# Kernel optimization log

Measured on AMD Instinct MI355X. Metric: run time of the kernel, lower is better.

Reference implementation:

```python
import jax, jax.numpy as jnp
import numpy as np

DIM = 4096
N_HEADS = 32
N_KV_HEADS = 8
HEAD_DIM = DIM // N_HEADS  # 128
KV_DIM = N_KV_HEADS * HEAD_DIM  # 1024
B, T = 2, 1024


def setup_inputs() -> dict:
    key = jax.random.key(0)
    ks = jax.random.split(key, 5)
    s1 = 1.0 / np.sqrt(DIM)
    return {
        "x": jax.random.normal(ks[0], (B, T, DIM), dtype=jnp.float32),
        "W1": jax.random.uniform(ks[1], (DIM + 2 * KV_DIM, DIM), dtype=jnp.float32, minval=-s1, maxval=s1),
        "b1": jax.random.uniform(ks[2], (DIM + 2 * KV_DIM,), dtype=jnp.float32, minval=-s1, maxval=s1),
        "W2": jax.random.uniform(ks[3], (DIM, DIM), dtype=jnp.float32, minval=-s1, maxval=s1),
        "b2": jax.random.uniform(ks[4], (DIM,), dtype=jnp.float32, minval=-s1, maxval=s1),
    }


def reference(x, W1, b1, W2, b2):
    Bn, Tn, D = x.shape
    G = N_HEADS // N_KV_HEADS
    qkv = x @ W1.T + b1  # [B,T,D+2*KV_DIM]
    q = qkv[:, :, :DIM]
    k = qkv[:, :, DIM:DIM + KV_DIM]
    v = qkv[:, :, DIM + KV_DIM:]
    # Faithful to torch repeat_interleave(G, dim=-1): scalar-level interleave on flat feature dim
    k = jnp.repeat(k, G, axis=-1)  # [B,T,D]
    v = jnp.repeat(v, G, axis=-1)
    q = q.reshape(Bn, Tn, N_HEADS, HEAD_DIM).transpose(0, 2, 1, 3)  # [B,H,T,hd]
    k = k.reshape(Bn, Tn, N_HEADS, HEAD_DIM).transpose(0, 2, 1, 3)
    v = v.reshape(Bn, Tn, N_HEADS, HEAD_DIM).transpose(0, 2, 1, 3)
    scale = 1.0 / jnp.sqrt(jnp.asarray(HEAD_DIM, dtype=x.dtype))
    qk = jnp.einsum('bhqd,bhkd->bhqk', q, k) * scale  # [B,H,T,T]
    causal = jnp.tril(jnp.ones((Tn, Tn), dtype=bool))
    qk = jnp.where(causal[None, None], qk, jnp.asarray(-jnp.inf, dtype=qk.dtype))
    att = jax.nn.softmax(qk, axis=-1)
    out = jnp.einsum('bhqk,bhkd->bhqd', att, v)  # [B,H,T,hd]
    out = out.transpose(0, 2, 1, 3).reshape(Bn, Tn, D)
    return out @ W2.T + b2
```

## Files before the change

kernel.cpp:

```cpp
#include <hip/hip_runtime.h>

#define DIMX  4096
#define NH    32
#define HD    128
#define BB    2
#define TT    1024
#define MROWS (BB*TT)
#define CQKV  3072
#define SCALE_Q 0.12751743f

typedef _Float16 half_t;
typedef __attribute__((ext_vector_type(4))) _Float16 f16x4;
typedef __attribute__((ext_vector_type(8))) _Float16 f16x8;
typedef __attribute__((ext_vector_type(4))) float    f32x4;

__device__ __forceinline__ void async_copy16(const void* gsrc, void* ldst) {
  __builtin_amdgcn_global_load_lds(
      (const __attribute__((address_space(1))) unsigned int*)gsrc,
      (__attribute__((address_space(3))) unsigned int*)ldst,
      16, 0, 0);
}

__global__ __launch_bounds__(256) void cvt_f32_f16_kernel(
    const float4* __restrict__ src, f16x4* __restrict__ dst, int n4) {
  int stride = gridDim.x * blockDim.x;
  for (int i = blockIdx.x * blockDim.x + threadIdx.x; i < n4; i += stride) {
    float4 f = src[i];
    f16x4 h;
    h.x = (_Float16)f.x; h.y = (_Float16)f.y;
    h.z = (_Float16)f.z; h.w = (_Float16)f.w;
    dst[i] = h;
  }
}

__global__ __launch_bounds__(256) void fold_w1_kernel(
    const float* __restrict__ W1, const float* __restrict__ b1,
    half_t* __restrict__ W1f, float* __restrict__ b1f)
{
  long idx = (long)blockIdx.x * 256 + threadIdx.x;
  int row = (int)(idx >> 10);
  int c4  = ((int)idx & 1023) << 2;
  f16x4 h;
  if (row < 1024) {
    const float* s = W1 + ((long)row << 2) * DIMX + c4;
    float4 a = *(const float4*)s;
    float4 b = *(const float4*)(s + DIMX);
    float4 c = *(const float4*)(s + 2 * DIMX);
    float4 d = *(const float4*)(s + 3 * DIMX);
    h.x = (_Float16)((a.x + b.x + c.x + d.x) * SCALE_Q);
    h.y = (_Float16)((a.y + b.y + c.y + d.y) * SCALE_Q);
    h.z = (_Float16)((a.z + b.z + c.z + d.z) * SCALE_Q);
    h.w = (_Float16)((a.w + b.w + c.w + d.w) * SCALE_Q);
    if (c4 == 0) {
      const float* bb = b1 + ((long)row << 2);
      b1f[row] = (bb[0] + bb[1] + bb[2] + bb[3]) * SCALE_Q;
    }
  } else {
    const float* s = W1 + ((long)(row + 3072)) * DIMX + c4;
    float4 a = *(const float4*)s;
    h.x = (_Float16)a.x; h.y = (_Float16)a.y;
    h.z = (_Float16)a.z; h.w = (_Float16)a.w;
    if (c4 == 0) b1f[row] = b1[row + 3072];
  }
  *(f16x4*)&W1f[(long)row * DIMX + c4] = h;
}

__global__ __launch_bounds__(256) void fold_w2_kernel(
    const float* __restrict__ W2, half_t* __restrict__ W2f)
{
  long idx = (long)blockIdx.x * 256 + threadIdx.x;
  int row = (int)(idx >> 8);
  int j4  = ((int)idx & 255) << 2;
  const float* s = W2 + (long)row * DIMX + ((long)j4 << 2);
  float4 a = *(const float4*)s;
  float4 b = *(const float4*)(s + 4);
  float4 c = *(const float4*)(s + 8);
  float4 d = *(const float4*)(s + 12);
  f16x4 h;
  h.x = (_Float16)(a.x + a.y + a.z + a.w);
  h.y = (_Float16)(b.x + b.y + b.z + b.w);
  h.z = (_Float16)(c.x + c.y + c.z + c.w);
  h.w = (_Float16)(d.x + d.y + d.z + d.w);
  *(f16x4*)&W2f[(long)row * 1024 + j4] = h;
}


__global__ __launch_bounds__(256, 3) void gemm_nt_splitk(
    const half_t* __restrict__ A, const half_t* __restrict__ Bw,
    float* __restrict__ Cp0, float* __restrict__ Cp1,
    int M, int N, int K)
{
  __shared__ alignas(16) half_t As[128 * 64];
  __shared__ alignas(16) half_t Bs[128 * 64];

  const int tid  = threadIdx.x;
  const int lane = tid & 63;
  const int w    = tid >> 6;
  const long row0 = (long)blockIdx.y * 128;
  const long col0 = (long)blockIdx.x * 128;
  const int  KH   = K >> 1;
  const long k0   = (long)blockIdx.z * KH;

  const int rr = tid >> 3;
  const int cs = (((tid & 7) ^ (rr & 7)) << 3);
  const half_t* ga[4]; const half_t* gb[4];
#pragma unroll
  for (int i = 0; i < 4; ++i) {
    ga[i] = A  + (row0 + i * 32 + rr) * K + k0 + cs;
    gb[i] = Bw + (col0 + i * 32 + rr) * K + k0 + cs;
  }
  half_t* lds_a = &As[w * 512];
  half_t* lds_b = &Bs[w * 512];

  const int wm = (w >> 1) * 64;
  const int wn = (w & 1) * 64;
  const int fr   = lane & 15;
  const int quad = lane >> 4;
  const int rsw  = fr & 7;
  const int o0 = ((quad ^ rsw) << 3);
  const int o1 = (((quad | 4) ^ rsw) << 3);
  const half_t* paw = &As[(wm + fr) * 64];
  const half_t* pbw = &Bs[(wn + fr) * 64];

  f32x4 acc[4][4] = {};

  for (int kt = 0; kt < KH; kt += 64) {
    __syncthreads();
#pragma unroll
    for (int i = 0; i < 4; ++i) async_copy16(ga[i] + kt, lds_a + i * 2048);
#pragma unroll
    for (int i = 0; i < 4; ++i) async_copy16(gb[i] + kt, lds_b + i * 2048);
    __syncthreads();

    f16x8 af[4], bf[4];
#pragma unroll
    for (int mi = 0; mi < 4; ++mi) af[mi] = *(const f16x8*)(paw + mi * 1024 + o0);
#pragma unroll
    for (int ni = 0; ni < 4; ++ni) bf[ni] = *(const f16x8*)(pbw + ni * 1024 + o0);
#pragma unroll
    for (int mi = 0; mi < 4; ++mi)
#pragma unroll
      for (int ni = 0; ni < 4; ++ni)
        acc[mi][ni] = __builtin_amdgcn_mfma_f32_16x16x32_f16(
            af[mi], bf[ni], acc[mi][ni], 0, 0, 0);

#pragma unroll
    for (int mi = 0; mi < 4; ++mi) af[mi] = *(const f16x8*)(paw + mi * 1024 + o1);
#pragma unroll
    for (int ni = 0; ni < 4; ++ni) bf[ni] = *(const f16x8*)(pbw + ni * 1024 + o1);
#pragma unroll
    for (int mi = 0; mi < 4; ++mi)
#pragma unroll
      for (int ni = 0; ni < 4; ++ni)
        acc[mi][ni] = __builtin_amdgcn_mfma_f32_16x16x32_f16(
            af[mi], bf[ni], acc[mi][ni], 0, 0, 0);
  }

  float* Cp = blockIdx.z ? Cp1 : Cp0;
  const int er = (lane >> 4) * 4;
  const int ec = lane & 15;
#pragma unroll
  for (int mi = 0; mi < 4; ++mi) {
#pragma unroll
    for (int ni = 0; ni < 4; ++ni) {
      long gn = col0 + wn + ni * 16 + ec;
#pragma unroll
      for (int r = 0; r < 4; ++r) {
        long gm = row0 + wm + mi * 16 + er + r;
        Cp[gm * N + gn] = acc[mi][ni][r];
      }
    }
  }
}

template<int OUT_IS_F16>
__global__ __launch_bounds__(256, 3) void gemm_nt_bias(
    const half_t* __restrict__ A, const half_t* __restrict__ Bw,
    const float* __restrict__ bias, void* __restrict__ Cout,
    int M, int N, int K)
{
  __shared__ alignas(16) half_t As[128 * 64];
  __shared__ alignas(16) half_t Bs[128 * 64];

  const int tid  = threadIdx.x;
  const int lane = tid & 63;
  const int w    = tid >> 6;
  const long row0 = (long)blockIdx.y * 128;
  const long col0 = (long)blockIdx.x * 128;

  const int rr = tid >> 3;
  const int cs = (((tid & 7) ^ (rr & 7)) << 3);
  const half_t* ga[4]; const half_t* gb[4];
#pragma unroll
  for (int i = 0; i < 4; ++i) {
    ga[i] = A  + (row0 + i * 32 + rr) * K + cs;
    gb[i] = Bw + (col0 + i * 32 + rr) * K + cs;
  }
  half_t* lds_a = &As[w * 512];
  half_t* lds_b = &Bs[w * 512];

  const int wm = (w >> 1) * 64;
  const int wn = (w & 1) * 64;
  const int fr   = lane & 15;
  const int quad = lane >> 4;
  const int rsw  = fr & 7;
  const int o0 = ((quad ^ rsw) << 3);
  const int o1 = (((quad | 4) ^ rsw) << 3);
  const half_t* paw = &As[(wm + fr) * 64];
  const half_t* pbw = &Bs[(wn + fr) * 64];

  f32x4 acc[4][4] = {};

  for (int kt = 0; kt < K; kt += 64) {
    __syncthreads();
#pragma unroll
    for (int i = 0; i < 4; ++i) async_copy16(ga[i] + kt, lds_a + i * 2048);
#pragma unroll
    for (int i = 0; i < 4; ++i) async_copy16(gb[i] + kt, lds_b + i * 2048);
    __syncthreads();

    f16x8 af[4], bf[4];
#pragma unroll
    for (int mi = 0; mi < 4; ++mi) af[mi] = *(const f16x8*)(paw + mi * 1024 + o0);
#pragma unroll
    for (int ni = 0; ni < 4; ++ni) bf[ni] = *(const f16x8*)(pbw + ni * 1024 + o0);
#pragma unroll
    for (int mi = 0; mi < 4; ++mi)
#pragma unroll
      for (int ni = 0; ni < 4; ++ni)
        acc[mi][ni] = __builtin_amdgcn_mfma_f32_16x16x32_f16(
            af[mi], bf[ni], acc[mi][ni], 0, 0, 0);

#pragma unroll
    for (int mi = 0; mi < 4; ++mi) af[mi] = *(const f16x8*)(paw + mi * 1024 + o1);
#pragma unroll
    for (int ni = 0; ni < 4; ++ni) bf[ni] = *(const f16x8*)(pbw + ni * 1024 + o1);
#pragma unroll
    for (int mi = 0; mi < 4; ++mi)
#pragma unroll
      for (int ni = 0; ni < 4; ++ni)
        acc[mi][ni] = __builtin_amdgcn_mfma_f32_16x16x32_f16(
            af[mi], bf[ni], acc[mi][ni], 0, 0, 0);
  }

  const int er = (lane >> 4) * 4;
  const int ec = lane & 15;
#pragma unroll
  for (int mi = 0; mi < 4; ++mi) {
#pragma unroll
    for (int ni = 0; ni < 4; ++ni) {
      long gn = col0 + wn + ni * 16 + ec;
      float bv = bias[gn];
#pragma unroll
      for (int r = 0; r < 4; ++r) {
        long gm = row0 + wm + mi * 16 + er + r;
        float v = acc[mi][ni][r] + bv;
        if (OUT_IS_F16) ((half_t*)Cout)[gm * N + gn] = (half_t)v;
        else            ((float*)Cout)[gm * N + gn]  = v;
      }
    }
  }
}

__global__ __launch_bounds__(256) void splitk_reduce_kernel(
    const float4* __restrict__ C0, const float4* __restrict__ C1,
    const float4* __restrict__ bias4, f16x4* __restrict__ dst)
{
  const int col  = blockIdx.x * 256 + threadIdx.x;
  const long row = blockIdx.y;
  const long i   = row * (CQKV / 4) + col;
  float4 a = C0[i];
  float4 b = C1[i];
  float4 bv = bias4[col];
  f16x4 h;
  h.x = (_Float16)(a.x + b.x + bv.x);
  h.y = (_Float16)(a.y + b.y + bv.y);
  h.z = (_Float16)(a.z + b.z + bv.z);
  h.w = (_Float16)(a.w + b.w + bv.w);
  dst[i] = h;
}

#define VTS 72
#define PSS 72
__global__ __launch_bounds__(256, 4) void attn_kernel(
    const half_t* __restrict__ qkv,
    half_t* __restrict__ attc)
{
  __shared__ alignas(16) half_t Ks[64 * 32];
  __shared__ alignas(16) half_t Vt[48 * VTS];
  __shared__ alignas(16) half_t Ps[4][16 * PSS];

  const int tid  = threadIdx.x;
  const int lane = tid & 63;
  const int w    = tid >> 6;
  const int low  = lane & 15;
  const int quad = lane >> 4;
  const int bh   = blockIdx.y;
  const int b    = bh >> 5;
  const int h    = bh & 31;
  const long rb  = (long)b * TT;

  if (tid < 8) {
    f16x8 one;
#pragma unroll
    for (int i = 0; i < 8; ++i) one[i] = (_Float16)1.0f;
    *(f16x8*)&Vt[32 * VTS + tid * 8] = one;
  }

  const int srow = tid >> 2;
  const int sc4  = (tid & 3) << 3;
  half_t* ksdst  = &Ks[w * 512];
  half_t* psw    = &Ps[w][0];
  float*  Ob     = (float*)psw;

  const int tile = blockIdx.x;
  const int t0   = tile * 64;
  const int qg   = t0 + 16 * w;

  f16x8 qf = *(const f16x8*)&qkv[(rb + qg + low) * CQKV + h * 32 + quad * 8];

  f32x4 acc0 = {}, acc1 = {}, acc2 = {};
  const f32x4 zero = {};

  for (int c = 0; c <= t0; c += 64) {
    __syncthreads();
    const half_t* kg = &qkv[(rb + c + srow) * CQKV + 1024 + h * 32 + sc4];
    async_copy16(kg, ksdst);
    f16x8 vv = *(const f16x8*)(kg + 1024);
#pragma unroll
    for (int j = 0; j < 8; ++j)
      Vt[(sc4 + j) * VTS + srow] = vv[j];
    __syncthreads();

    f32x4 s[4];
#pragma unroll
    for (int st = 0; st < 4; ++st) {
      f16x8 kf = *(const f16x8*)&Ks[(st * 16 + low) * 32 + quad * 8];
      s[st] = __builtin_amdgcn_mfma_f32_16x16x32_f16(qf, kf, zero, 0, 0, 0);
    }

    const bool diag = (c == t0);
#pragma unroll
    for (int st = 0; st < 4; ++st) {
#pragma unroll
      for (int r = 0; r < 4; ++r) {
        const int key = c + st * 16 + low;
        const int q   = qg + 4 * quad + r;
        float p = __builtin_amdgcn_exp2f(s[st][r]);
        if (diag && key > q) p = 0.f;
        psw[(4 * quad + r) * PSS + st * 16 + low] = (_Float16)p;
      }
    }

    f16x8 p0 = *(const f16x8*)&psw[low * PSS + 0 * 32 + quad * 8];
    f16x8 p1 = *(const f16x8*)&psw[low * PSS + 1 * 32 + quad * 8];

    f16x8 v00 = *(const f16x8*)&Vt[(0  + low) * VTS + 0  + quad * 8];
    f16x8 v01 = *(const f16x8*)&Vt[(0  + low) * VTS + 32 + quad * 8];
    f16x8 v10 = *(const f16x8*)&Vt[(16 + low) * VTS + 0  + quad * 8];
    f16x8 v11 = *(const f16x8*)&Vt[(16 + low) * VTS + 32 + quad * 8];
    f16x8 v20 = *(const f16x8*)&Vt[(32 + low) * VTS + 0  + quad * 8];
    f16x8 v21 = *(const f16x8*)&Vt[(32 + low) * VTS + 32 + quad * 8];

    acc0 = __builtin_amdgcn_mfma_f32_16x16x32_f16(v00, p0, acc0, 0, 0, 0);
    acc0 = __builtin_amdgcn_mfma_f32_16x16x32_f16(v01, p1, acc0, 0, 0, 0);
    acc1 = __builtin_amdgcn_mfma_f32_16x16x32_f16(v10, p0, acc1, 0, 0, 0);
    acc1 = __builtin_amdgcn_mfma_f32_16x16x32_f16(v11, p1, acc1, 0, 0, 0);
    acc2 = __builtin_amdgcn_mfma_f32_16x16x32_f16(v20, p0, acc2, 0, 0, 0);
    acc2 = __builtin_amdgcn_mfma_f32_16x16x32_f16(v21, p1, acc2, 0, 0, 0);
  }

  __syncthreads();

  float linv = 1.0f / __shfl(acc2[0], low);

#pragma unroll
  for (int r = 0; r < 4; ++r) {
    Ob[low * 36 + 0  + 4 * quad + r] = acc0[r] * linv;
    Ob[low * 36 + 16 + 4 * quad + r] = acc1[r] * linv;
  }
  __syncthreads();

  f16x8 ov;
#pragma unroll
  for (int i = 0; i < 8; ++i)
    ov[i] = (_Float16)Ob[low * 36 + quad * 8 + i];
  *(f16x8*)&attc[(rb + qg + low) * 1024 + h * 32 + quad * 8] = ov;
}

extern "C" void kernel_launch(void* const* d_in, const int* in_sizes, int n_in,
                              void* d_out, int out_size, void* d_ws, size_t ws_size,
                              hipStream_t stream) {
  (void)in_sizes; (void)n_in; (void)out_size; (void)ws_size;
  const float* x  = (const float*)d_in[0];
  const float* W1 = (const float*)d_in[1];
  const float* b1 = (const float*)d_in[2];
  const float* W2 = (const float*)d_in[3];
  const float* b2 = (const float*)d_in[4];
  float* out = (float*)d_out;

  const size_t nX   = (size_t)MROWS * DIMX;
  const size_t nW1f = (size_t)CQKV  * DIMX;
  const size_t nW2f = (size_t)DIMX  * 1024;
  const size_t nQKV = (size_t)MROWS * CQKV;
  const size_t nATT = (size_t)MROWS * 1024;

  half_t* ws   = (half_t*)d_ws;
  half_t* xh   = ws;
  half_t* w1f  = xh   + nX;
  half_t* w2f  = w1f  + nW1f;
  half_t* qkvc = w2f  + nW2f;
  half_t* attc = qkvc + nQKV;
  float*  b1f  = (float*)(attc + nATT);
  float*  c1   = (float*)(b1f + 4096);

  cvt_f32_f16_kernel<<<4096, 256, 0, stream>>>((const float4*)x, (f16x4*)xh,
                                               (int)(nX / 4));
  fold_w1_kernel<<<12288, 256, 0, stream>>>(W1, b1, w1f, b1f);
  fold_w2_kernel<<<4096, 256, 0, stream>>>(W2, w2f);

  gemm_nt_splitk<<<dim3(CQKV / 128, MROWS / 128, 2), 256, 0, stream>>>(
      xh, w1f, out , c1 , MROWS, CQKV, DIMX);
  splitk_reduce_kernel<<<dim3(CQKV / 4 / 256, MROWS), 256, 0, stream>>>(
      (const float4*)out, (const float4*)c1, (const float4*)b1f,
      (f16x4*)qkvc);

  attn_kernel<<<dim3(16, BB * NH), 256, 0, stream>>>(qkvc, attc);

  gemm_nt_bias<0><<<dim3(DIMX / 128, MROWS / 128), 256, 0, stream>>>(
      attc, w2f, b2, (void*)out, MROWS, DIMX, 1024);
}
```

Baseline: 344.0 us.

## Pre-transpose V into a workspace and async-load swizzled K/V tiles in attention

Adds a separate kernel that transposes the V slice of the QKV buffer into a [b, d, t] layout, reusing the x-half workspace. The attention kernel then loads both K and V tiles straight into LDS with async global-to-LDS copies and XOR-swizzled layouts, replacing the per-thread scalar V transpose writes. The softmax row-sum MFMA now takes a constant ones register operand instead of a ones row in LDS. The cost is an extra kernel launch plus the V-transpose traffic, in exchange for less LDS write work and fewer bank conflicts inside the attention loop.

Result: slower. 352.1 us (+2.4%).

```diff
diff --git a/kernel.cpp b/kernel.cpp
--- a/kernel.cpp
+++ b/kernel.cpp
@@ -280,14 +280,41 @@
   dst[i] = h;
 }
 
-#define VTS 72
+__global__ __launch_bounds__(256) void v_transpose_kernel(
+    const half_t* __restrict__ qkvc, half_t* __restrict__ vt)
+{
+  __shared__ half_t lt[64][72];
+  const int t  = threadIdx.x;
+  const int b  = blockIdx.z;
+  const int d0 = blockIdx.x * 64;
+  const int k0 = blockIdx.y * 64;
+  const int tl = t >> 3;
+  const int dc = (t & 7) * 8;
+
+  const half_t* src = qkvc + ((long)b * TT + k0 + tl) * CQKV + 2048 + d0 + dc;
+  *(f16x8*)&lt[tl][dc]      = *(const f16x8*)src;
+  *(f16x8*)&lt[tl + 32][dc] = *(const f16x8*)(src + 32 * CQKV);
+  __syncthreads();
+
+  half_t* dstp = vt + ((long)b * 1024 + d0 + tl) * 1024 + k0 + dc;
+  f16x8 o0, o1;
+#pragma unroll
+  for (int j = 0; j < 8; ++j) {
+    o0[j] = lt[dc + j][tl];
+    o1[j] = lt[dc + j][tl + 32];
+  }
+  *(f16x8*)dstp = o0;
+  *(f16x8*)(dstp + 32 * 1024) = o1;
+}
+
 #define PSS 72
 __global__ __launch_bounds__(256, 4) void attn_kernel(
     const half_t* __restrict__ qkv,
+    const half_t* __restrict__ vt,
     half_t* __restrict__ attc)
 {
-  __shared__ alignas(16) half_t Ks[64 * 32];
-  __shared__ alignas(16) half_t Vt[48 * VTS];
+  __shared__ alignas(16) half_t Ks[32 * 64];
+  __shared__ alignas(16) half_t Vs[32 * 64];
   __shared__ alignas(16) half_t Ps[4][16 * PSS];
 
   const int tid  = threadIdx.x;
@@ -300,18 +327,16 @@
   const int h    = bh & 31;
   const long rb  = (long)b * TT;
 
-  if (tid < 8) {
-    f16x8 one;
-#pragma unroll
-    for (int i = 0; i < 8; ++i) one[i] = (_Float16)1.0f;
-    *(f16x8*)&Vt[32 * VTS + tid * 8] = one;
-  }
-
-  const int srow = tid >> 2;
-  const int sc4  = (tid & 3) << 3;
-  half_t* ksdst  = &Ks[w * 512];
-  half_t* psw    = &Ps[w][0];
-  float*  Ob     = (float*)psw;
+  const int su  = tid >> 3;
+  const int sp  = tid & 7;
+  const int spx = sp ^ (su & 7);
+  const half_t* kg = qkv + (rb + 2 * su + (spx >> 2)) * CQKV + 1024
+                         + h * 32 + (spx & 3) * 8;
+  const half_t* vg = vt + ((long)b * 1024 + h * 32 + su) * 1024 + spx * 8;
+  half_t* kdst = &Ks[w * 512];
+  half_t* vdst = &Vs[w * 512];
+  half_t* psw  = &Ps[w][0];
+  float*  Ob   = (float*)psw;
 
   const int tile = blockIdx.x;
   const int t0   = tile * 64;
@@ -319,23 +344,28 @@
 
   f16x8 qf = *(const f16x8*)&qkv[(rb + qg + low) * CQKV + h * 32 + quad * 8];
 
+  f16x8 onesf;
+#pragma unroll
+  for (int i = 0; i < 8; ++i) onesf[i] = (_Float16)1.0f;
+
   f32x4 acc0 = {}, acc1 = {}, acc2 = {};
   const f32x4 zero = {};
 
+  const int dsw = low & 7;
+  const int ksw = (low >> 1) & 7;
+  const int kp  = (((low & 1) << 2) | quad) ^ ksw;
+
   for (int c = 0; c <= t0; c += 64) {
     __syncthreads();
-    const half_t* kg = &qkv[(rb + c + srow) * CQKV + 1024 + h * 32 + sc4];
-    async_copy16(kg, ksdst);
-    f16x8 vv = *(const f16x8*)(kg + 1024);
-#pragma unroll
-    for (int j = 0; j < 8; ++j)
-      Vt[(sc4 + j) * VTS + srow] = vv[j];
+    async_copy16(kg + (long)c * CQKV, kdst);
+    async_copy16(vg + c, vdst);
     __syncthreads();
 
     f32x4 s[4];
 #pragma unroll
     for (int st = 0; st < 4; ++st) {
-      f16x8 kf = *(const f16x8*)&Ks[(st * 16 + low) * 32 + quad * 8];
+      const int u = st * 8 + (low >> 1);
+      f16x8 kf = *(const f16x8*)&Ks[u * 64 + kp * 8];
       s[st] = __builtin_amdgcn_mfma_f32_16x16x32_f16(qf, kf, zero, 0, 0, 0);
     }
 
@@ -355,24 +385,22 @@
     f16x8 p0 = *(const f16x8*)&psw[low * PSS + 0 * 32 + quad * 8];
     f16x8 p1 = *(const f16x8*)&psw[low * PSS + 1 * 32 + quad * 8];
 
-    f16x8 v00 = *(const f16x8*)&Vt[(0  + low) * VTS + 0  + quad * 8];
-    f16x8 v01 = *(const f16x8*)&Vt[(0  + low) * VTS + 32 + quad * 8];
-    f16x8 v10 = *(const f16x8*)&Vt[(16 + low) * VTS + 0  + quad * 8];
-    f16x8 v11 = *(const f16x8*)&Vt[(16 + low) * VTS + 32 + quad * 8];
-    f16x8 v20 = *(const f16x8*)&Vt[(32 + low) * VTS + 0  + quad * 8];
-    f16x8 v21 = *(const f16x8*)&Vt[(32 + low) * VTS + 32 + quad * 8];
-
-    acc0 = __builtin_amdgcn_mfma_f32_16x16x32_f16(v00, p0, acc0, 0, 0, 0);
-    acc0 = __builtin_amdgcn_mfma_f32_16x16x32_f16(v01, p1, acc0, 0, 0, 0);
-    acc1 = __builtin_amdgcn_mfma_f32_16x16x32_f16(v10, p0, acc1, 0, 0, 0);
-    acc1 = __builtin_amdgcn_mfma_f32_16x16x32_f16(v11, p1, acc1, 0, 0, 0);
-    acc2 = __builtin_amdgcn_mfma_f32_16x16x32_f16(v20, p0, acc2, 0, 0, 0);
-    acc2 = __builtin_amdgcn_mfma_f32_16x16x32_f16(v21, p1, acc2, 0, 0, 0);
+    f16x8 v00 = *(const f16x8*)&Vs[(0  + low) * 64 + ((0 + quad) ^ dsw) * 8];
+    f16x8 v01 = *(const f16x8*)&Vs[(0  + low) * 64 + ((4 + quad) ^ dsw) * 8];
+    f16x8 v10 = *(const f16x8*)&Vs[(16 + low) * 64 + ((0 + quad) ^ dsw) * 8];
+    f16x8 v11 = *(const f16x8*)&Vs[(16 + low) * 64 + ((4 + quad) ^ dsw) * 8];
+
+    acc0 = __builtin_amdgcn_mfma_f32_16x16x32_f16(v00,   p0, acc0, 0, 0, 0);
+    acc0 = __builtin_amdgcn_mfma_f32_16x16x32_f16(v01,   p1, acc0, 0, 0, 0);
+    acc1 = __builtin_amdgcn_mfma_f32_16x16x32_f16(v10,   p0, acc1, 0, 0, 0);
+    acc1 = __builtin_amdgcn_mfma_f32_16x16x32_f16(v11,   p1, acc1, 0, 0, 0);
+    acc2 = __builtin_amdgcn_mfma_f32_16x16x32_f16(onesf, p0, acc2, 0, 0, 0);
+    acc2 = __builtin_amdgcn_mfma_f32_16x16x32_f16(onesf, p1, acc2, 0, 0, 0);
   }
 
   __syncthreads();
 
-  float linv = 1.0f / __shfl(acc2[0], low);
+  float linv = 1.0f / acc2[0];
 
 #pragma unroll
   for (int r = 0; r < 4; ++r) {
@@ -413,6 +441,7 @@
   half_t* attc = qkvc + nQKV;
   float*  b1f  = (float*)(attc + nATT);
   float*  c1   = (float*)(b1f + 4096);
+  half_t* vt   = xh;
 
   cvt_f32_f16_kernel<<<4096, 256, 0, stream>>>((const float4*)x, (f16x4*)xh,
                                                (int)(nX / 4));
@@ -425,7 +454,9 @@
       (const float4*)out, (const float4*)c1, (const float4*)b1f,
       (f16x4*)qkvc);
 
-  attn_kernel<<<dim3(16, BB * NH), 256, 0, stream>>>(qkvc, attc);
+  v_transpose_kernel<<<dim3(16, 16, BB), 256, 0, stream>>>(qkvc, vt);
+
+  attn_kernel<<<dim3(16, BB * NH), 256, 0, stream>>>(qkvc, vt, attc);
 
   gemm_nt_bias<0><<<dim3(DIMX / 128, MROWS / 128), 256, 0, stream>>>(
       attc, w2f, b2, (void*)out, MROWS, DIMX, 1024);
```
